# Performance work log

Hardware: AMD Instinct MI355X
Metric: run time of the kernel (lower is better)

## Reference

```python
import jax, jax.numpy as jnp
import numpy as np

N_NODES = 100000
N_EDGES = 600000
NUM_GRAPHS = 512
IN_DIM = 128
HID = 64
HEADS = 2
NEG_SLOPE = 0.2


def gat_layer(h_in, src, dst, W, a_s, a_d, b, n_nodes):
    # W: [F_in, H*C], a_s/a_d: [H, C], b: [H*C]
    H, C = a_s.shape
    h = (h_in @ W).reshape(n_nodes, H, C)            # [N,H,C]
    alpha_src = jnp.einsum('nhc,hc->nh', h, a_s)      # [N,H]
    alpha_dst = jnp.einsum('nhc,hc->nh', h, a_d)      # [N,H]
    e = alpha_src[src] + alpha_dst[dst]               # [E,H]
    e = jnp.where(e >= 0, e, NEG_SLOPE * e)           # leaky_relu
    # segment softmax over destination node
    m = jax.ops.segment_max(e, dst, num_segments=n_nodes)
    m = jnp.where(jnp.isfinite(m), m, 0.0)
    ex = jnp.exp(e - m[dst])                          # [E,H]
    denom = jax.ops.segment_sum(ex, dst, num_segments=n_nodes)
    alpha = ex / jnp.maximum(denom[dst], 1e-16)       # [E,H]
    out = jax.ops.segment_sum(alpha[:, :, None] * h[src], dst, num_segments=n_nodes)
    return out.reshape(n_nodes, H * C) + b


def setup_inputs() -> dict:
    key = jax.random.key(0)
    ks = jax.random.split(key, 16)
    x = jax.random.normal(ks[0], (N_NODES, IN_DIM), dtype=jnp.float32)
    edge_index = jax.random.randint(ks[1], (2, N_EDGES), 0, N_NODES, dtype=jnp.int32)
    batch = jnp.sort(jax.random.randint(ks[2], (N_NODES,), 0, NUM_GRAPHS, dtype=jnp.int32))
    s = lambda *d: 1.0 / np.sqrt(d[0])
    W1 = jax.random.normal(ks[3], (IN_DIM, HEADS * HID), jnp.float32) * s(IN_DIM)
    a_src1 = jax.random.normal(ks[4], (HEADS, HID), jnp.float32) * s(HID)
    a_dst1 = jax.random.normal(ks[5], (HEADS, HID), jnp.float32) * s(HID)
    b1 = jnp.zeros((HEADS * HID,), jnp.float32)
    W2 = jax.random.normal(ks[6], (HEADS * HID, HID), jnp.float32) * s(HEADS * HID)
    a_src2 = jax.random.normal(ks[7], (1, HID), jnp.float32) * s(HID)
    a_dst2 = jax.random.normal(ks[8], (1, HID), jnp.float32) * s(HID)
    b2 = jnp.zeros((HID,), jnp.float32)
    Wf1 = jax.random.normal(ks[9], (2 * HID, HID), jnp.float32) * s(2 * HID)
    bf1 = jnp.zeros((HID,), jnp.float32)
    Wf2 = jax.random.normal(ks[10], (HID, 1), jnp.float32) * s(HID)
    bf2 = jnp.zeros((1,), jnp.float32)
    return dict(x=x, edge_index=edge_index, batch=batch, W1=W1, a_src1=a_src1,
                a_dst1=a_dst1, b1=b1, W2=W2, a_src2=a_src2, a_dst2=a_dst2, b2=b2,
                Wf1=Wf1, bf1=bf1, Wf2=Wf2, bf2=bf2)


def reference(x, edge_index, batch, W1, a_src1, a_dst1, b1, W2, a_src2, a_dst2, b2,
              Wf1, bf1, Wf2, bf2):
    n = x.shape[0]
    loops = jnp.arange(n, dtype=edge_index.dtype)
    src = jnp.concatenate([edge_index[0], loops])
    dst = jnp.concatenate([edge_index[1], loops])
    h = gat_layer(x, src, dst, W1, a_src1, a_dst1, b1, n)
    h = jax.nn.relu(h)
    h = gat_layer(h, src, dst, W2, a_src2, a_dst2, b2, n)  # [N, HID]
    # global mean + max pool per graph
    ones = jnp.ones((n,), h.dtype)
    counts = jax.ops.segment_sum(ones, batch, num_segments=NUM_GRAPHS)  # [G]
    mean = jax.ops.segment_sum(h, batch, num_segments=NUM_GRAPHS) / jnp.maximum(counts, 1.0)[:, None]
    mx = jax.ops.segment_max(h, batch, num_segments=NUM_GRAPHS)
    mx = jnp.where(counts[:, None] > 0, mx, 0.0)
    pooled = jnp.concatenate([mean, mx], axis=1)  # [G, 2*HID]
    out = jax.nn.relu(pooled @ Wf1 + bf1) @ Wf2 + bf2  # [G, 1]
    return out
```

## Files before the change

kernel.cpp:

```cpp
#include <hip/hip_runtime.h>

#define N_NODESC 100000
#define N_EDGESC 600000
#define E_TOTC   700000
#define NUM_GRAPHSC 512
#define NEG_SLOPE 0.2f
#define NEG_INF_ENC 0x007FFFFFu
#define SCAN_NB 128

typedef unsigned short ushort_t;
typedef __attribute__((ext_vector_type(8))) short bf16x8;
typedef __attribute__((ext_vector_type(4))) float f32x4;

__device__ __forceinline__ unsigned enc_f32(float f) {
    unsigned u = __float_as_uint(f);
    return (u & 0x80000000u) ? ~u : (u | 0x80000000u);
}
__device__ __forceinline__ float dec_f32(unsigned u) {
    u = (u & 0x80000000u) ? (u ^ 0x80000000u) : ~u;
    return __uint_as_float(u);
}
__device__ __forceinline__ ushort_t f32_to_bf16(float f) {
    unsigned u = __float_as_uint(f);
    return (ushort_t)((u + 0x7FFFu + ((u >> 16) & 1u)) >> 16);
}
__device__ __forceinline__ float bf16_to_f32(ushort_t h) {
    return __uint_as_float(((unsigned)h) << 16);
}
__device__ __forceinline__ unsigned pack_bf16x2(float a, float b) {
    return (unsigned)f32_to_bf16(a) | ((unsigned)f32_to_bf16(b) << 16);
}

__device__ __forceinline__ void glds16(const void* g, void* l) {
    __builtin_amdgcn_global_load_lds(
        (const __attribute__((address_space(1))) void*)g,
        (__attribute__((address_space(3))) void*)l, 16, 0, 0);
}

__global__ __launch_bounds__(256) void init_all(float* __restrict__ msum,
                                                unsigned* __restrict__ mmax,
                                                float* __restrict__ cnt,
                                                int* __restrict__ deg,
                                                const float* __restrict__ W1,
                                                const float* __restrict__ W2,
                                                ushort_t* __restrict__ wPre1,
                                                ushort_t* __restrict__ wPre2) {
    int i = blockIdx.x * 256 + threadIdx.x;
    if (i < NUM_GRAPHSC * 64) { msum[i] = 0.f; mmax[i] = NEG_INF_ENC; }
    if (i < NUM_GRAPHSC) cnt[i] = 0.f;
    if (i < N_NODESC) deg[i] = 0;
    if (i < 128 * 128) {
        int n = i >> 7, k = i & 127;
        wPre1[n * 128 + k] = f32_to_bf16(W1[k * 128 + n]);
    } else if (i < 128 * 128 + 64 * 128) {
        int j = i - 128 * 128;
        int n = j >> 7, k = j & 127;
        wPre2[n * 128 + k] = f32_to_bf16(W2[k * 64 + n]);
    }
}

__global__ __launch_bounds__(256) void hist_dst(const int* __restrict__ ei,
                                                int* __restrict__ deg) {
    int e = blockIdx.x * blockDim.x + threadIdx.x;
    if (e >= E_TOTC) return;
    int d = (e < N_EDGESC) ? ei[N_EDGESC + e] : e - N_EDGESC;
    atomicAdd(&deg[d], 1);
}

__global__ __launch_bounds__(256) void scan_partial(const int* __restrict__ deg,
                                                    int* __restrict__ bsum, int n) {
    __shared__ int red[256];
    int chunk = (n + SCAN_NB - 1) / SCAN_NB;
    int lo = blockIdx.x * chunk, hi = min(lo + chunk, n);
    int s = 0;
    for (int i = lo + threadIdx.x; i < hi; i += 256) s += deg[i];
    red[threadIdx.x] = s;
    __syncthreads();
    for (int d = 128; d; d >>= 1) {
        if (threadIdx.x < d) red[threadIdx.x] += red[threadIdx.x + d];
        __syncthreads();
    }
    if (threadIdx.x == 0) bsum[blockIdx.x] = red[0];
}

__global__ __launch_bounds__(256) void scan_final(const int* __restrict__ deg,
                                                  const int* __restrict__ bsum,
                                                  int* __restrict__ off, int n) {
    __shared__ int bs[SCAN_NB];
    __shared__ int tile[256];
    __shared__ int carry;
    int t = threadIdx.x;
    if (t < SCAN_NB) bs[t] = bsum[t];
    __syncthreads();
    for (int d = 1; d < SCAN_NB; d <<= 1) {
        int v = (t >= d && t < SCAN_NB) ? bs[t - d] : 0;
        __syncthreads();
        if (t < SCAN_NB) bs[t] += v;
        __syncthreads();
    }
    if (t == 0) carry = blockIdx.x ? bs[blockIdx.x - 1] : 0;
    __syncthreads();
    int chunk = (n + SCAN_NB - 1) / SCAN_NB;
    int lo = blockIdx.x * chunk, hi = min(lo + chunk, n);
    for (int base = lo; base < hi; base += 256) {
        int i = base + t;
        int v = (i < hi) ? deg[i] : 0;
        tile[t] = v;
        __syncthreads();
        for (int d = 1; d < 256; d <<= 1) {
            int u = (t >= d) ? tile[t - d] : 0;
            __syncthreads();
            tile[t] += u;
            __syncthreads();
        }
        if (i < hi) off[i] = carry + tile[t] - v;
        __syncthreads();
        if (t == 0) carry += tile[255];
        __syncthreads();
    }
}

__global__ __launch_bounds__(256) void scatter_csr(const int* __restrict__ ei,
                                                   int* __restrict__ off,
                                                   int* __restrict__ csr) {
    int e = blockIdx.x * blockDim.x + threadIdx.x;
    if (e >= E_TOTC) return;
    int s, d;
    if (e < N_EDGESC) { s = ei[e]; d = ei[N_EDGESC + e]; } else { s = d = e - N_EDGESC; }
    int slot = atomicAdd(&off[d], 1);
    csr[slot] = s;
}

__global__ __launch_bounds__(256) void gemm1_mfma(const float* __restrict__ X,
                                                  const ushort_t* __restrict__ Wp,
                                                  const float* __restrict__ a_s,
                                                  const float* __restrict__ a_d,
                                                  float* __restrict__ as_out,
                                                  float* __restrict__ ad_out,
                                                  ushort_t* __restrict__ Y16, int N) {
    __shared__ float sx[64 * 128];
    int tid = threadIdx.x;
    int wave = tid >> 6, lane = tid & 63;
    int quad = lane >> 4, l16 = lane & 15;
    size_t node0 = (size_t)blockIdx.x * 64 + (size_t)wave * 16;

    {
        int rhalf = lane >> 5;
        int cb = (lane & 31) * 16;
#pragma unroll
        for (int c = 0; c < 8; ++c) {
            int rl = 2 * c + rhalf;
            size_t grow = node0 + rl;
            if (grow >= (size_t)N) grow = N - 1;
            int goff = cb ^ ((rl & 15) << 4);
            glds16((const char*)(X + grow * 128) + goff,
                   (char*)sx + wave * 8192 + c * 1024);
        }
    }
    asm volatile("s_waitcnt vmcnt(0)" ::: "memory");
    __builtin_amdgcn_sched_barrier(0);

    const char* swx = (const char*)sx + wave * 8192 + l16 * 512;
    int skey = (l16 & 15) << 4;

    f32x4 acc[8];
#pragma unroll
    for (int ct = 0; ct < 8; ++ct) acc[ct] = (f32x4){0.f, 0.f, 0.f, 0.f};

#pragma unroll
    for (int kc = 0; kc < 4; ++kc) {
        int b = kc * 128 + quad * 32;
        float4 xa = *(const float4*)(swx + (b ^ skey));
        float4 xb = *(const float4*)(swx + ((b + 16) ^ skey));
        union { bf16x8 v; unsigned u[4]; } af;
        af.u[0] = pack_bf16x2(xa.x, xa.y);
        af.u[1] = pack_bf16x2(xa.z, xa.w);
        af.u[2] = pack_bf16x2(xb.x, xb.y);
        af.u[3] = pack_bf16x2(xb.z, xb.w);
#pragma unroll
        for (int ct = 0; ct < 8; ++ct) {
            bf16x8 bb = *(const bf16x8*)(Wp + (size_t)(ct * 16 + l16) * 128 + kc * 32 + quad * 8);
            acc[ct] = __builtin_amdgcn_mfma_f32_16x16x32_bf16(af.v, bb, acc[ct], 0, 0, 0);
        }
    }

    unsigned* Yu = (unsigned*)Y16;
    float asv0[4], asv1[4], adv0[4], adv1[4];
#pragma unroll
    for (int ct = 0; ct < 4; ++ct) {
        int c = ct * 16 + l16;
        asv0[ct] = a_s[c]; asv1[ct] = a_s[64 + c];
        adv0[ct] = a_d[c]; adv1[ct] = a_d[64 + c];
    }
#pragma unroll
    for (int r = 0; r < 4; ++r) {
        size_t row = node0 + quad * 4 + r;
        bool ok = row < (size_t)N;
        if (ok) {
#pragma unroll
            for (int ct = 0; ct < 4; ++ct)
                Yu[row * 64 + ct * 16 + l16] = pack_bf16x2(acc[ct][r], acc[ct + 4][r]);
        }
        float ps0 = 0.f, pd0 = 0.f, ps1 = 0.f, pd1 = 0.f;
#pragma unroll
        for (int ct = 0; ct < 4; ++ct) {
            ps0 += acc[ct][r] * asv0[ct];     pd0 += acc[ct][r] * adv0[ct];
            ps1 += acc[ct + 4][r] * asv1[ct]; pd1 += acc[ct + 4][r] * adv1[ct];
        }
#pragma unroll
        for (int sh = 1; sh < 16; sh <<= 1) {
            ps0 += __shfl_xor(ps0, sh); pd0 += __shfl_xor(pd0, sh);
            ps1 += __shfl_xor(ps1, sh); pd1 += __shfl_xor(pd1, sh);
        }
        if (l16 == 0 && ok) {
            *(float2*)(as_out + row * 2) = make_float2(ps0, ps1);
            *(float2*)(ad_out + row * 2) = make_float2(pd0, pd1);
        }
    }
}

__global__ __launch_bounds__(256) void gemm2_mfma(const ushort_t* __restrict__ Xb,
                                                  const ushort_t* __restrict__ Wp,
                                                  const float* __restrict__ a_s,
                                                  const float* __restrict__ a_d,
                                                  float* __restrict__ as_out,
                                                  float* __restrict__ ad_out,
                                                  ushort_t* __restrict__ Y16, int N) {
    __shared__ ushort_t sx[64 * 128];
    int tid = threadIdx.x;
    int wave = tid >> 6, lane = tid & 63;
    int quad = lane >> 4, l16 = lane & 15;
    size_t node0 = (size_t)blockIdx.x * 64 + (size_t)wave * 16;

    {
        int rq = lane >> 4;
        int cb = (lane & 15) * 16;
#pragma unroll
        for (int c = 0; c < 4; ++c) {
            int rl = 4 * c + rq;
            size_t grow = node0 + rl;
            if (grow >= (size_t)N) grow = N - 1;
            int goff = cb ^ ((rl & 15) << 4);
            glds16((const char*)(Xb + grow * 128) + goff,
                   (char*)sx + wave * 4096 + c * 1024);
        }
    }
    asm volatile("s_waitcnt vmcnt(0)" ::: "memory");
    __builtin_amdgcn_sched_barrier(0);

    const char* swx = (const char*)sx + wave * 4096 + l16 * 256;
    int skey = (l16 & 15) << 4;

    f32x4 acc[4];
#pragma unroll
    for (int ct = 0; ct < 4; ++ct) acc[ct] = (f32x4){0.f, 0.f, 0.f, 0.f};

#pragma unroll
    for (int kc = 0; kc < 4; ++kc) {
        int b = kc * 64 + quad * 16;
        bf16x8 a = *(const bf16x8*)(swx + (b ^ skey));
#pragma unroll
        for (int ct = 0; ct < 4; ++ct) {
            bf16x8 bb = *(const bf16x8*)(Wp + (size_t)(ct * 16 + l16) * 128 + kc * 32 + quad * 8);
            acc[ct] = __builtin_amdgcn_mfma_f32_16x16x32_bf16(a, bb, acc[ct], 0, 0, 0);
        }
    }

    float asv[4], adv[4];
#pragma unroll
    for (int ct = 0; ct < 4; ++ct) { asv[ct] = a_s[ct * 16 + l16]; adv[ct] = a_d[ct * 16 + l16]; }
#pragma unroll
    for (int r = 0; r < 4; ++r) {
        size_t row = node0 + quad * 4 + r;
        bool ok = row < (size_t)N;
        if (ok) {
#pragma unroll
            for (int ct = 0; ct < 4; ++ct)
                Y16[row * 64 + ct * 16 + l16] = f32_to_bf16(acc[ct][r]);
        }
        float ps = acc[0][r] * asv[0] + acc[1][r] * asv[1] +
                   acc[2][r] * asv[2] + acc[3][r] * asv[3];
        float pd = acc[0][r] * adv[0] + acc[1][r] * adv[1] +
                   acc[2][r] * adv[2] + acc[3][r] * adv[3];
#pragma unroll
        for (int sh = 1; sh < 16; sh <<= 1) {
            ps += __shfl_xor(ps, sh);
            pd += __shfl_xor(pd, sh);
        }
        if (l16 == 0 && ok) { as_out[row] = ps; ad_out[row] = pd; }
    }
}

template <int H, bool RELU, bool OB16>
__global__ __launch_bounds__(256) void gat_gather(const int* __restrict__ off_end,
                                                  const int* __restrict__ deg,
                                                  const int* __restrict__ csr,
                                                  const float* __restrict__ as,
                                                  const float* __restrict__ ad,
                                                  const ushort_t* __restrict__ H16,
                                                  const float* __restrict__ b,
                                                  void* __restrict__ outp, int N) {
    int lane = threadIdx.x & 63;
    int wave = threadIdx.x >> 6;
    int l = lane & 15;
    int gbase = lane & 48;
    int n = blockIdx.x * 16 + wave * 4 + (lane >> 4);
    if (n >= N) return;
    int dg = deg[n];
    int o = off_end[n] - dg;
    float adv[H];
#pragma unroll
    for (int h = 0; h < H; ++h) adv[h] = ad[n * H + h];

    float acc[H][4], den[H];
#pragma unroll
    for (int h = 0; h < H; ++h) {
        den[h] = 0.f;
#pragma unroll
        for (int q = 0; q < 4; ++q) acc[h][q] = 0.f;
    }

    const unsigned* Hu = (const unsigned*)H16;

    for (int base = 0; base < dg; base += 16) {
        int i = base + l;
        bool valid = i < dg;
        int s = valid ? csr[o + i] : 0;
        float v[H];
        if (H == 2) {
            float2 p = valid ? ((const float2*)as)[s] : make_float2(0.f, 0.f);
            v[0] = p.x + adv[0];
            v[H - 1] = p.y + adv[H - 1];
        } else {
            v[0] = valid ? as[s] + adv[0] : 0.f;
        }
#pragma unroll
        for (int h = 0; h < H; ++h) {
            float e = v[h] >= 0.f ? v[h] : NEG_SLOPE * v[h];
            v[h] = valid ? __expf(e) : 0.f;
            den[h] += v[h];
        }
        int wpk = (H == 2) ? (int)pack_bf16x2(v[0], v[H - 1])
                           : (int)__float_as_uint(v[0]);
        int cnt = min(dg - base, 16);
        int cnt4 = (cnt + 3) & ~3;
        for (int j = 0; j < cnt4; j += 4) {
#pragma unroll
            for (int u = 0; u < 4; ++u) {
                int src = gbase + j + u;
                int sj = __shfl(s, src);
                int wp = __shfl(wpk, src);
                if (H == 2) {
                    float w0 = __uint_as_float(((unsigned)wp) << 16);
                    float w1 = __uint_as_float(((unsigned)wp) & 0xffff0000u);
                    uint4 hu = *(const uint4*)(Hu + (size_t)sj * 64 + l * 4);
                    acc[0][0] += w0 * __uint_as_float(hu.x << 16);
                    acc[H - 1][0] += w1 * __uint_as_float(hu.x & 0xffff0000u);
                    acc[0][1] += w0 * __uint_as_float(hu.y << 16);
                    acc[H - 1][1] += w1 * __uint_as_float(hu.y & 0xffff0000u);
                    acc[0][2] += w0 * __uint_as_float(hu.z << 16);
                    acc[H - 1][2] += w1 * __uint_as_float(hu.z & 0xffff0000u);
                    acc[0][3] += w0 * __uint_as_float(hu.w << 16);
                    acc[H - 1][3] += w1 * __uint_as_float(hu.w & 0xffff0000u);
                } else {
                    float w0 = __uint_as_float((unsigned)wp);
                    uint2 hu = *(const uint2*)((const unsigned*)(H16 + (size_t)sj * 64) + l * 2);
                    acc[0][0] += w0 * __uint_as_float(hu.x << 16);
                    acc[0][1] += w0 * __uint_as_float(hu.x & 0xffff0000u);
                    acc[0][2] += w0 * __uint_as_float(hu.y << 16);
                    acc[0][3] += w0 * __uint_as_float(hu.y & 0xffff0000u);
                }
            }
        }
    }
#pragma unroll
    for (int h = 0; h < H; ++h) {
#pragma unroll
        for (int sh = 8; sh; sh >>= 1) den[h] += __shfl_xor(den[h], sh);
    }
    if (H == 2) {
        float4 b0 = *(const float4*)(b + l * 4);
        float4 b1 = *(const float4*)(b + 64 + l * 4);
        float r0[4], r1[4];
        float id0 = 1.f / fmaxf(den[0], 1e-16f);
        float id1 = 1.f / fmaxf(den[H - 1], 1e-16f);
        r0[0] = acc[0][0] * id0 + b0.x; r0[1] = acc[0][1] * id0 + b0.y;
        r0[2] = acc[0][2] * id0 + b0.z; r0[3] = acc[0][3] * id0 + b0.w;
        r1[0] = acc[H - 1][0] * id1 + b1.x; r1[1] = acc[H - 1][1] * id1 + b1.y;
        r1[2] = acc[H - 1][2] * id1 + b1.z; r1[3] = acc[H - 1][3] * id1 + b1.w;
        if (RELU) {
#pragma unroll
            for (int q = 0; q < 4; ++q) { r0[q] = fmaxf(r0[q], 0.f); r1[q] = fmaxf(r1[q], 0.f); }
        }
        ushort_t* outb = (ushort_t*)outp;
        uint2 p0 = make_uint2(pack_bf16x2(r0[0], r0[1]), pack_bf16x2(r0[2], r0[3]));
        uint2 p1 = make_uint2(pack_bf16x2(r1[0], r1[1]), pack_bf16x2(r1[2], r1[3]));
        *(uint2*)(outb + (size_t)n * 128 + l * 4) = p0;
        *(uint2*)(outb + (size_t)n * 128 + 64 + l * 4) = p1;
    } else {
        float4 bv = *(const float4*)(b + l * 4);
        float id0 = 1.f / fmaxf(den[0], 1e-16f);
        float4 r;
        r.x = acc[0][0] * id0 + bv.x; r.y = acc[0][1] * id0 + bv.y;
        r.z = acc[0][2] * id0 + bv.z; r.w = acc[0][3] * id0 + bv.w;
        if (RELU) { r.x = fmaxf(r.x, 0.f); r.y = fmaxf(r.y, 0.f);
                    r.z = fmaxf(r.z, 0.f); r.w = fmaxf(r.w, 0.f); }
        *(float4*)((float*)outp + (size_t)n * 64 + l * 4) = r;
    }
}

__global__ __launch_bounds__(256) void pool_nodes(const float* __restrict__ h2,
                                                  const int* __restrict__ batch,
                                                  float* __restrict__ msum,
                                                  unsigned* __restrict__ mmax,
                                                  float* __restrict__ cnt, int N) {
    int wid = threadIdx.x >> 6, lane = threadIdx.x & 63;
    int n0 = (blockIdx.x * 4 + wid) * 64;
    if (n0 >= N) return;
    int n1 = min(n0 + 64, N);
    int curg = batch[n0];
    float s = 0.f, m = -1e30f;
    int c = 0;
    for (int n = n0; n < n1; ++n) {
        int g = batch[n];
        float v = h2[(size_t)n * 64 + lane];
        if (g != curg) {
            atomicAdd(&msum[curg * 64 + lane], s);
            atomicMax(&mmax[curg * 64 + lane], enc_f32(m));
            if (lane == 0) atomicAdd(&cnt[curg], (float)c);
            s = 0.f; m = -1e30f; c = 0; curg = g;
        }
        s += v;
        m = fmaxf(m, v);
        ++c;
    }
    atomicAdd(&msum[curg * 64 + lane], s);
    atomicMax(&mmax[curg * 64 + lane], enc_f32(m));
    if (lane == 0) atomicAdd(&cnt[curg], (float)c);
}

__global__ __launch_bounds__(64) void mlp_head(const float* __restrict__ msum,
                                               const unsigned* __restrict__ mmax,
                                               const float* __restrict__ cnt,
                                               const float* __restrict__ Wf1,
                                               const float* __restrict__ bf1,
                                               const float* __restrict__ Wf2,
                                               const float* __restrict__ bf2,
                                               float* __restrict__ out) {
    __shared__ float pooled[128];
    int g = blockIdx.x, lane = threadIdx.x;
    float c = cnt[g];
    pooled[lane] = msum[g * 64 + lane] / fmaxf(c, 1.0f);
    pooled[64 + lane] = (c > 0.f) ? dec_f32(mmax[g * 64 + lane]) : 0.f;
    __syncthreads();
    float acc = bf1[lane];
#pragma unroll
    for (int k = 0; k < 128; ++k) acc += pooled[k] * Wf1[k * 64 + lane];
    acc = fmaxf(acc, 0.f);
    float r = acc * Wf2[lane];
#pragma unroll
    for (int off = 32; off; off >>= 1) r += __shfl_xor(r, off);
    if (lane == 0) out[g] = r + bf2[0];
}

extern "C" void kernel_launch(void* const* d_in, const int* in_sizes, int n_in,
                              void* d_out, int out_size, void* d_ws, size_t ws_size,
                              hipStream_t stream) {
    const float* x    = (const float*)d_in[0];
    const int*   ei   = (const int*)d_in[1];
    const int*   batch= (const int*)d_in[2];
    const float* W1   = (const float*)d_in[3];
    const float* as1  = (const float*)d_in[4];
    const float* ad1  = (const float*)d_in[5];
    const float* b1   = (const float*)d_in[6];
    const float* W2   = (const float*)d_in[7];
    const float* as2  = (const float*)d_in[8];
    const float* ad2  = (const float*)d_in[9];
    const float* b2   = (const float*)d_in[10];
    const float* Wf1  = (const float*)d_in[11];
    const float* bf1  = (const float*)d_in[12];
    const float* Wf2  = (const float*)d_in[13];
    const float* bf2  = (const float*)d_in[14];
    float* out = (float*)d_out;

    const size_t N = N_NODESC;
    float* ws = (float*)d_ws;
    ushort_t* h16_1 = (ushort_t*)ws;
    ushort_t* out1b = (ushort_t*)(ws + N * 64);
    ushort_t* h16_2 = (ushort_t*)(ws + N * 128);
    float*    out2  = ws + N * 160;
    float*    small = ws + N * 224;
    float*    as1b = small;
    float*    ad1b = small + 2 * N;
    float*    as2b = small + 4 * N;
    float*    ad2b = small + 5 * N;
    float*    msum = small + 6 * N;
    unsigned* mmax = (unsigned*)(small + 6 * N + 512 * 64);
    float*    cntb = small + 6 * N + 2 * 512 * 64;
    int* ip  = (int*)(small + 6 * N + 2 * 512 * 64 + 512);
    int* deg  = ip;
    int* off  = ip + N;
    int* csr  = ip + 2 * N;
    int* bsum = ip + 2 * N + E_TOTC;
    ushort_t* wPre1 = (ushort_t*)(bsum + SCAN_NB);
    ushort_t* wPre2 = wPre1 + 128 * 128;

    init_all<<<(N_NODESC + 255) / 256, 256, 0, stream>>>(msum, mmax, cntb, deg,
                                                         W1, W2, wPre1, wPre2);

    hist_dst<<<(E_TOTC + 255) / 256, 256, 0, stream>>>(ei, deg);
    scan_partial<<<SCAN_NB, 256, 0, stream>>>(deg, bsum, N);
    scan_final<<<SCAN_NB, 256, 0, stream>>>(deg, bsum, off, N);
    scatter_csr<<<(E_TOTC + 255) / 256, 256, 0, stream>>>(ei, off, csr);

    const int NBLK64 = (N_NODESC + 63) / 64;
    const int NBLK16 = (N_NODESC + 15) / 16;

    gemm1_mfma<<<NBLK64, 256, 0, stream>>>(x, wPre1, as1, ad1, as1b, ad1b, h16_1, N);
    gat_gather<2, true, true><<<NBLK16, 256, 0, stream>>>(off, deg, csr, as1b,
                                                          ad1b, h16_1, b1, out1b, N);

    gemm2_mfma<<<NBLK64, 256, 0, stream>>>(out1b, wPre2, as2, ad2, as2b, ad2b, h16_2, N);
    gat_gather<1, false, false><<<NBLK16, 256, 0, stream>>>(off, deg, csr, as2b,
                                                            ad2b, h16_2, b2, out2, N);

    pool_nodes<<<(N + 255) / 256, 256, 0, stream>>>(out2, batch, msum, mmax, cntb, N);
    mlp_head<<<NUM_GRAPHSC, 64, 0, stream>>>(msum, mmax, cntb, Wf1, bf1, Wf2, bf2, out);
}
```

Before: 305.1 us.

## Make node GEMMs persistent with double-buffered async LDS prefetch

Both projection GEMM kernels become persistent: 512 blocks whose waves stride over 16-row tiles. Each wave prefetches its next tile into a second LDS buffer via async global-to-LDS loads while it computes the current tile, using partial vmcnt waits. This aims to hide global load latency and amortize launch and setup cost, such as loading the attention vectors once per wave. In exchange, LDS per block doubles and the total wave count drops. The kernels also now depend on vmcnt accounting being correct, and any other outstanding loads would break that accounting.

```diff
diff --git a/kernel.cpp b/kernel.cpp
--- a/kernel.cpp
+++ b/kernel.cpp
@@ -138,15 +138,21 @@
                                                   float* __restrict__ as_out,
                                                   float* __restrict__ ad_out,
                                                   ushort_t* __restrict__ Y16, int N) {
-    __shared__ float sx[64 * 128];
+    __shared__ float sx[2][4][2048];
     int tid = threadIdx.x;
     int wave = tid >> 6, lane = tid & 63;
     int quad = lane >> 4, l16 = lane & 15;
-    size_t node0 = (size_t)blockIdx.x * 64 + (size_t)wave * 16;
+
+    const int NT = (N + 15) / 16;
+    const int TSTRIDE = 512 * 4;
+    int tau = blockIdx.x * 4 + wave;
+    if (tau >= NT) return;
+
+    int rhalf = lane >> 5;
+    int cb = (lane & 31) * 16;
 
     {
-        int rhalf = lane >> 5;
-        int cb = (lane & 31) * 16;
+        size_t node0 = (size_t)tau * 16;
 #pragma unroll
         for (int c = 0; c < 8; ++c) {
             int rl = 2 * c + rhalf;
@@ -154,37 +160,10 @@
             if (grow >= (size_t)N) grow = N - 1;
             int goff = cb ^ ((rl & 15) << 4);
             glds16((const char*)(X + grow * 128) + goff,
-                   (char*)sx + wave * 8192 + c * 1024);
-        }
-    }
-    asm volatile("s_waitcnt vmcnt(0)" ::: "memory");
-    __builtin_amdgcn_sched_barrier(0);
-
-    const char* swx = (const char*)sx + wave * 8192 + l16 * 512;
-    int skey = (l16 & 15) << 4;
-
-    f32x4 acc[8];
-#pragma unroll
-    for (int ct = 0; ct < 8; ++ct) acc[ct] = (f32x4){0.f, 0.f, 0.f, 0.f};
-
-#pragma unroll
-    for (int kc = 0; kc < 4; ++kc) {
-        int b = kc * 128 + quad * 32;
-        float4 xa = *(const float4*)(swx + (b ^ skey));
-        float4 xb = *(const float4*)(swx + ((b + 16) ^ skey));
-        union { bf16x8 v; unsigned u[4]; } af;
-        af.u[0] = pack_bf16x2(xa.x, xa.y);
-        af.u[1] = pack_bf16x2(xa.z, xa.w);
-        af.u[2] = pack_bf16x2(xb.x, xb.y);
-        af.u[3] = pack_bf16x2(xb.z, xb.w);
-#pragma unroll
-        for (int ct = 0; ct < 8; ++ct) {
-            bf16x8 bb = *(const bf16x8*)(Wp + (size_t)(ct * 16 + l16) * 128 + kc * 32 + quad * 8);
-            acc[ct] = __builtin_amdgcn_mfma_f32_16x16x32_bf16(af.v, bb, acc[ct], 0, 0, 0);
-        }
-    }
-
-    unsigned* Yu = (unsigned*)Y16;
+                   (char*)&sx[0][wave][0] + c * 1024);
+        }
+    }
+
     float asv0[4], asv1[4], adv0[4], adv1[4];
 #pragma unroll
     for (int ct = 0; ct < 4; ++ct) {
@@ -192,30 +171,79 @@
         asv0[ct] = a_s[c]; asv1[ct] = a_s[64 + c];
         adv0[ct] = a_d[c]; adv1[ct] = a_d[64 + c];
     }
-#pragma unroll
-    for (int r = 0; r < 4; ++r) {
-        size_t row = node0 + quad * 4 + r;
-        bool ok = row < (size_t)N;
-        if (ok) {
-#pragma unroll
-            for (int ct = 0; ct < 4; ++ct)
-                Yu[row * 64 + ct * 16 + l16] = pack_bf16x2(acc[ct][r], acc[ct + 4][r]);
-        }
-        float ps0 = 0.f, pd0 = 0.f, ps1 = 0.f, pd1 = 0.f;
-#pragma unroll
-        for (int ct = 0; ct < 4; ++ct) {
-            ps0 += acc[ct][r] * asv0[ct];     pd0 += acc[ct][r] * adv0[ct];
-            ps1 += acc[ct + 4][r] * asv1[ct]; pd1 += acc[ct + 4][r] * adv1[ct];
-        }
-#pragma unroll
-        for (int sh = 1; sh < 16; sh <<= 1) {
-            ps0 += __shfl_xor(ps0, sh); pd0 += __shfl_xor(pd0, sh);
-            ps1 += __shfl_xor(ps1, sh); pd1 += __shfl_xor(pd1, sh);
-        }
-        if (l16 == 0 && ok) {
-            *(float2*)(as_out + row * 2) = make_float2(ps0, ps1);
-            *(float2*)(ad_out + row * 2) = make_float2(pd0, pd1);
-        }
+    unsigned* Yu = (unsigned*)Y16;
+    int skey = (l16 & 15) << 4;
+    int buf = 0;
+
+    for (; tau < NT; tau += TSTRIDE) {
+        int tnext = tau + TSTRIDE;
+        if (tnext < NT) {
+            size_t node0n = (size_t)tnext * 16;
+#pragma unroll
+            for (int c = 0; c < 8; ++c) {
+                int rl = 2 * c + rhalf;
+                size_t grow = node0n + rl;
+                if (grow >= (size_t)N) grow = N - 1;
+                int goff = cb ^ ((rl & 15) << 4);
+                glds16((const char*)(X + grow * 128) + goff,
+                       (char*)&sx[buf ^ 1][wave][0] + c * 1024);
+            }
+            asm volatile("s_waitcnt vmcnt(8)" ::: "memory");
+        } else {
+            asm volatile("s_waitcnt vmcnt(0)" ::: "memory");
+        }
+        __builtin_amdgcn_sched_barrier(0);
+
+        size_t node0 = (size_t)tau * 16;
+        const char* swx = (const char*)&sx[buf][wave][0] + l16 * 512;
+
+        f32x4 acc[8];
+#pragma unroll
+        for (int ct = 0; ct < 8; ++ct) acc[ct] = (f32x4){0.f, 0.f, 0.f, 0.f};
+
+#pragma unroll
+        for (int kc = 0; kc < 4; ++kc) {
+            int b = kc * 128 + quad * 32;
+            float4 xa = *(const float4*)(swx + (b ^ skey));
+            float4 xb = *(const float4*)(swx + ((b + 16) ^ skey));
+            union { bf16x8 v; unsigned u[4]; } af;
+            af.u[0] = pack_bf16x2(xa.x, xa.y);
+            af.u[1] = pack_bf16x2(xa.z, xa.w);
+            af.u[2] = pack_bf16x2(xb.x, xb.y);
+            af.u[3] = pack_bf16x2(xb.z, xb.w);
+#pragma unroll
+            for (int ct = 0; ct < 8; ++ct) {
+                bf16x8 bb = *(const bf16x8*)(Wp + (size_t)(ct * 16 + l16) * 128 + kc * 32 + quad * 8);
+                acc[ct] = __builtin_amdgcn_mfma_f32_16x16x32_bf16(af.v, bb, acc[ct], 0, 0, 0);
+            }
+        }
+
+#pragma unroll
+        for (int r = 0; r < 4; ++r) {
+            size_t row = node0 + quad * 4 + r;
+            bool ok = row < (size_t)N;
+            if (ok) {
+#pragma unroll
+                for (int ct = 0; ct < 4; ++ct)
+                    Yu[row * 64 + ct * 16 + l16] = pack_bf16x2(acc[ct][r], acc[ct + 4][r]);
+            }
+            float ps0 = 0.f, pd0 = 0.f, ps1 = 0.f, pd1 = 0.f;
+#pragma unroll
+            for (int ct = 0; ct < 4; ++ct) {
+                ps0 += acc[ct][r] * asv0[ct];     pd0 += acc[ct][r] * adv0[ct];
+                ps1 += acc[ct + 4][r] * asv1[ct]; pd1 += acc[ct + 4][r] * adv1[ct];
+            }
+#pragma unroll
+            for (int sh = 1; sh < 16; sh <<= 1) {
+                ps0 += __shfl_xor(ps0, sh); pd0 += __shfl_xor(pd0, sh);
+                ps1 += __shfl_xor(ps1, sh); pd1 += __shfl_xor(pd1, sh);
+            }
+            if (l16 == 0 && ok) {
+                *(float2*)(as_out + row * 2) = make_float2(ps0, ps1);
+                *(float2*)(ad_out + row * 2) = make_float2(pd0, pd1);
+            }
+        }
+        buf ^= 1;
     }
 }
 
@@ -226,15 +254,21 @@
                                                   float* __restrict__ as_out,
                                                   float* __restrict__ ad_out,
                                                   ushort_t* __restrict__ Y16, int N) {
-    __shared__ ushort_t sx[64 * 128];
+    __shared__ ushort_t sx[2][4][2048];
     int tid = threadIdx.x;
     int wave = tid >> 6, lane = tid & 63;
     int quad = lane >> 4, l16 = lane & 15;
-    size_t node0 = (size_t)blockIdx.x * 64 + (size_t)wave * 16;
+
+    const int NT = (N + 15) / 16;
+    const int TSTRIDE = 512 * 4;
+    int tau = blockIdx.x * 4 + wave;
+    if (tau >= NT) return;
+
+    int rq = lane >> 4;
+    int cb = (lane & 15) * 16;
 
     {
-        int rq = lane >> 4;
-        int cb = (lane & 15) * 16;
+        size_t node0 = (size_t)tau * 16;
 #pragma unroll
         for (int c = 0; c < 4; ++c) {
             int rl = 4 * c + rq;
@@ -242,52 +276,74 @@
             if (grow >= (size_t)N) grow = N - 1;
             int goff = cb ^ ((rl & 15) << 4);
             glds16((const char*)(Xb + grow * 128) + goff,
-                   (char*)sx + wave * 4096 + c * 1024);
-        }
-    }
-    asm volatile("s_waitcnt vmcnt(0)" ::: "memory");
-    __builtin_amdgcn_sched_barrier(0);
-
-    const char* swx = (const char*)sx + wave * 4096 + l16 * 256;
+                   (char*)&sx[0][wave][0] + c * 1024);
+        }
+    }
+
+    float asv[4], adv[4];
+#pragma unroll
+    for (int ct = 0; ct < 4; ++ct) { asv[ct] = a_s[ct * 16 + l16]; adv[ct] = a_d[ct * 16 + l16]; }
     int skey = (l16 & 15) << 4;
-
-    f32x4 acc[4];
-#pragma unroll
-    for (int ct = 0; ct < 4; ++ct) acc[ct] = (f32x4){0.f, 0.f, 0.f, 0.f};
-
-#pragma unroll
-    for (int kc = 0; kc < 4; ++kc) {
-        int b = kc * 64 + quad * 16;
-        bf16x8 a = *(const bf16x8*)(swx + (b ^ skey));
-#pragma unroll
-        for (int ct = 0; ct < 4; ++ct) {
-            bf16x8 bb = *(const bf16x8*)(Wp + (size_t)(ct * 16 + l16) * 128 + kc * 32 + quad * 8);
-            acc[ct] = __builtin_amdgcn_mfma_f32_16x16x32_bf16(a, bb, acc[ct], 0, 0, 0);
-        }
-    }
-
-    float asv[4], adv[4];
-#pragma unroll
-    for (int ct = 0; ct < 4; ++ct) { asv[ct] = a_s[ct * 16 + l16]; adv[ct] = a_d[ct * 16 + l16]; }
-#pragma unroll
-    for (int r = 0; r < 4; ++r) {
-        size_t row = node0 + quad * 4 + r;
-        bool ok = row < (size_t)N;
-        if (ok) {
-#pragma unroll
-            for (int ct = 0; ct < 4; ++ct)
-                Y16[row * 64 + ct * 16 + l16] = f32_to_bf16(acc[ct][r]);
-        }
-        float ps = acc[0][r] * asv[0] + acc[1][r] * asv[1] +
-                   acc[2][r] * asv[2] + acc[3][r] * asv[3];
-        float pd = acc[0][r] * adv[0] + acc[1][r] * adv[1] +
-                   acc[2][r] * adv[2] + acc[3][r] * adv[3];
-#pragma unroll
-        for (int sh = 1; sh < 16; sh <<= 1) {
-            ps += __shfl_xor(ps, sh);
-            pd += __shfl_xor(pd, sh);
-        }
-        if (l16 == 0 && ok) { as_out[row] = ps; ad_out[row] = pd; }
+    int buf = 0;
+
+    for (; tau < NT; tau += TSTRIDE) {
+        int tnext = tau + TSTRIDE;
+        if (tnext < NT) {
+            size_t node0n = (size_t)tnext * 16;
+#pragma unroll
+            for (int c = 0; c < 4; ++c) {
+                int rl = 4 * c + rq;
+                size_t grow = node0n + rl;
+                if (grow >= (size_t)N) grow = N - 1;
+                int goff = cb ^ ((rl & 15) << 4);
+                glds16((const char*)(Xb + grow * 128) + goff,
+                       (char*)&sx[buf ^ 1][wave][0] + c * 1024);
+            }
+            asm volatile("s_waitcnt vmcnt(4)" ::: "memory");
+        } else {
+            asm volatile("s_waitcnt vmcnt(0)" ::: "memory");
+        }
+        __builtin_amdgcn_sched_barrier(0);
+
+        size_t node0 = (size_t)tau * 16;
+        const char* swx = (const char*)&sx[buf][wave][0] + l16 * 256;
+
+        f32x4 acc[4];
+#pragma unroll
+        for (int ct = 0; ct < 4; ++ct) acc[ct] = (f32x4){0.f, 0.f, 0.f, 0.f};
+
+#pragma unroll
+        for (int kc = 0; kc < 4; ++kc) {
+            int b = kc * 64 + quad * 16;
+            bf16x8 a = *(const bf16x8*)(swx + (b ^ skey));
+#pragma unroll
+            for (int ct = 0; ct < 4; ++ct) {
+                bf16x8 bb = *(const bf16x8*)(Wp + (size_t)(ct * 16 + l16) * 128 + kc * 32 + quad * 8);
+                acc[ct] = __builtin_amdgcn_mfma_f32_16x16x32_bf16(a, bb, acc[ct], 0, 0, 0);
+            }
+        }
+
+#pragma unroll
+        for (int r = 0; r < 4; ++r) {
+            size_t row = node0 + quad * 4 + r;
+            bool ok = row < (size_t)N;
+            if (ok) {
+#pragma unroll
+                for (int ct = 0; ct < 4; ++ct)
+                    Y16[row * 64 + ct * 16 + l16] = f32_to_bf16(acc[ct][r]);
+            }
+            float ps = acc[0][r] * asv[0] + acc[1][r] * asv[1] +
+                       acc[2][r] * asv[2] + acc[3][r] * asv[3];
+            float pd = acc[0][r] * adv[0] + acc[1][r] * adv[1] +
+                       acc[2][r] * adv[2] + acc[3][r] * adv[3];
+#pragma unroll
+            for (int sh = 1; sh < 16; sh <<= 1) {
+                ps += __shfl_xor(ps, sh);
+                pd += __shfl_xor(pd, sh);
+            }
+            if (l16 == 0 && ok) { as_out[row] = ps; ad_out[row] = pd; }
+        }
+        buf ^= 1;
     }
 }
 
@@ -513,14 +569,14 @@
     scan_final<<<SCAN_NB, 256, 0, stream>>>(deg, bsum, off, N);
     scatter_csr<<<(E_TOTC + 255) / 256, 256, 0, stream>>>(ei, off, csr);
 
-    const int NBLK64 = (N_NODESC + 63) / 64;
+    const int NBLKP  = 512;
     const int NBLK16 = (N_NODESC + 15) / 16;
 
-    gemm1_mfma<<<NBLK64, 256, 0, stream>>>(x, wPre1, as1, ad1, as1b, ad1b, h16_1, N);
+    gemm1_mfma<<<NBLKP, 256, 0, stream>>>(x, wPre1, as1, ad1, as1b, ad1b, h16_1, N);
     gat_gather<2, true, true><<<NBLK16, 256, 0, stream>>>(off, deg, csr, as1b,
                                                           ad1b, h16_1, b1, out1b, N);
 
-    gemm2_mfma<<<NBLK64, 256, 0, stream>>>(out1b, wPre2, as2, ad2, as2b, ad2b, h16_2, N);
+    gemm2_mfma<<<NBLKP, 256, 0, stream>>>(out1b, wPre2, as2, ad2, as2b, ad2b, h16_2, N);
     gat_gather<1, false, false><<<NBLK16, 256, 0, stream>>>(off, deg, csr, as2b,
                                                             ad2b, h16_2, b2, out2, N);
 
```

After: 308.2 us. About the same (+1.0%).
